# Kernel tuning notes

Measured on AMD Instinct MI355X. Metric: run time of the kernel, lower is better.

Reference implementation:

```python
import jax, jax.numpy as jnp
import numpy as np

SIGNAL = (32, 32)
KERNEL = (8, 8)
N_FEATURES = [64, 128, 128]
BATCH = 64
ALPHA = 0.5          # source references an undefined global `alpha`; fixed here
LEAKY_SLOPE = 0.01   # torch F.leaky_relu default


def _join_tensor(S, K, loc):
    i = np.arange(S)[:, None, None]
    j = np.arange(S)[None, :, None]
    k = np.arange(K)[None, None, :]
    M = (j >= i) & (i == np.maximum(j, k + loc))
    return jnp.asarray(M.astype(np.float32))


def _meet_tensor(S, K, loc):
    i = np.arange(S)[:, None, None]
    j = np.arange(S)[None, :, None]
    k = np.arange(K)[None, None, :]
    M = (j >= i) & (i == np.minimum(j, k + loc))
    return jnp.asarray(M.astype(np.float32))


def setup_inputs() -> dict:
    key = jax.random.key(0)
    sx, sy = SIGNAL
    kx, ky = KERNEL
    # meet layers use kernel_loc = signal - kernel; join layers use (0, 0)
    cmx = _meet_tensor(sx, kx, sx - kx)
    cmy = _meet_tensor(sy, ky, sy - ky)
    cjx = _join_tensor(sx, kx, 0)
    cjy = _join_tensor(sy, ky, 0)

    keys = jax.random.split(key, 16)
    x = jax.random.normal(keys[0], (BATCH, N_FEATURES[0], sx, sy), dtype=jnp.float32)

    def kaiming(k, shape):
        fan_in = shape[0] * shape[1] * shape[2]  # kx*ky*in_features
        return jax.random.normal(k, shape, dtype=jnp.float32) * np.float32(np.sqrt(2.0 / fan_in))

    inp = {"x": x, "cmx": cmx, "cmy": cmy, "cjx": cjx, "cjy": cjy}
    for li in range(len(N_FEATURES) - 1):
        fi, fo = N_FEATURES[li], N_FEATURES[li + 1]
        inp[f"mw{li}"] = kaiming(keys[1 + 2 * li], (kx, ky, fi, fo))
        inp[f"mb{li}"] = jnp.zeros((fo, 1, 1), dtype=jnp.float32)
        inp[f"jw{li}"] = kaiming(keys[2 + 2 * li], (kx, ky, fi, fo))
        inp[f"jb{li}"] = jnp.zeros((fo, 1, 1), dtype=jnp.float32)
    return inp


def _lattice_conv(cx, cy, X, W, b):
    # Y[m,g,x,y] = sum_{i,j,a,b} cx[i,x,a] cy[j,y,b] X[m,f,i,j] W[a,b,f,g] + bias
    return jnp.einsum('ixa,jyb,mfij,abfg->mgxy', cx, cy, X, W, optimize='optimal') + b


def reference(x, cmx, cmy, cjx, cjy, mw0, mb0, jw0, jb0, mw1, mb1, jw1, jb1):
    params = [(mw0, mb0, jw0, jb0), (mw1, mb1, jw1, jb1)]
    for mw, mb, jw, jb in params:
        m = _lattice_conv(cmx, cmy, x, mw, mb)
        j = _lattice_conv(cjx, cjy, x, jw, jb)
        x = jax.nn.leaky_relu((1.0 - ALPHA) * m + ALPHA * j, negative_slope=LEAKY_SLOPE)
    return x
```

## Files before the change

### kernel.cpp

```cpp
#include <hip/hip_runtime.h>
#include <stdint.h>


typedef __attribute__((ext_vector_type(8))) short short8;
typedef __attribute__((ext_vector_type(4))) float floatx4;

__device__ __forceinline__ float bf2f(unsigned short u) {
  union { uint32_t u; float f; } c; c.u = ((uint32_t)u) << 16; return c.f;
}
__device__ __forceinline__ unsigned short f2bf(float f) {
  union { float f; uint32_t u; } c; c.f = f;
  uint32_t u = c.u;
  uint32_t r = (u + 0x7FFFu + ((u >> 16) & 1u)) >> 16;
  return (unsigned short)r;
}

__global__ void detect_and_bias(const unsigned short* __restrict__ xa,
                                const void* __restrict__ mb0,
                                const void* __restrict__ jb0,
                                const void* __restrict__ mb1,
                                const void* __restrict__ jb1,
                                float* __restrict__ bias0,
                                float* __restrict__ bias1,
                                int* __restrict__ flag) {
  __shared__ int cnt;
  if (threadIdx.x == 0) cnt = 0;
  __syncthreads();
  unsigned short v = xa[threadIdx.x];
  int e = (v >> 7) & 0xFF;
  int ok = (v == 0) || (e >= 110 && e <= 140);
  atomicAdd(&cnt, ok);
  __syncthreads();
  int fp32 = (cnt >= 240) ? 0 : 1;
  if (threadIdx.x == 0) *flag = fp32;
  int g = threadIdx.x & 127;
  const void* mb = (threadIdx.x < 128) ? mb0 : mb1;
  const void* jb = (threadIdx.x < 128) ? jb0 : jb1;
  float* bo = (threadIdx.x < 128) ? bias0 : bias1;
  float m = fp32 ? ((const float*)mb)[g] : bf2f(((const unsigned short*)mb)[g]);
  float j = fp32 ? ((const float*)jb)[g] : bf2f(((const unsigned short*)jb)[g]);
  bo[g] = 0.5f * (m + j);
}

__global__ __launch_bounds__(256) void transpose_in(
    const unsigned short* __restrict__ s16, const float* __restrict__ s32,
    unsigned short* __restrict__ dst, int R, int C,
    const int* __restrict__ flag) {
  __shared__ unsigned short tile[32][33];
  int fp32 = *flag;
  int tx = threadIdx.x, ty = threadIdx.y;
  int c0 = blockIdx.x * 32, r0 = blockIdx.y * 32;
  if (fp32) {
#pragma unroll
    for (int i = 0; i < 32; i += 8)
      tile[ty + i][tx] = f2bf(s32[(size_t)(r0 + ty + i) * C + (c0 + tx)]);
  } else {
#pragma unroll
    for (int i = 0; i < 32; i += 8)
      tile[ty + i][tx] = s16[(size_t)(r0 + ty + i) * C + (c0 + tx)];
  }
  __syncthreads();
#pragma unroll
  for (int i = 0; i < 32; i += 8)
    dst[(size_t)(c0 + ty + i) * R + (r0 + tx)] = tile[tx][ty + i];
}

__global__ __launch_bounds__(256) void transpose_out(
    const unsigned short* __restrict__ src, unsigned short* __restrict__ d16,
    float* __restrict__ d32, int R, int C, const int* __restrict__ flag) {
  __shared__ unsigned short tile[32][33];
  int fp32 = *flag;
  int tx = threadIdx.x, ty = threadIdx.y;
  int c0 = blockIdx.x * 32, r0 = blockIdx.y * 32;
#pragma unroll
  for (int i = 0; i < 32; i += 8)
    tile[ty + i][tx] = src[(size_t)(r0 + ty + i) * C + (c0 + tx)];
  __syncthreads();
  if (fp32) {
#pragma unroll
    for (int i = 0; i < 32; i += 8)
      d32[(size_t)(c0 + ty + i) * R + (r0 + tx)] = bf2f(tile[tx][ty + i]);
  } else {
#pragma unroll
    for (int i = 0; i < 32; i += 8)
      d16[(size_t)(c0 + ty + i) * R + (r0 + tx)] = tile[tx][ty + i];
  }
}

__global__ __launch_bounds__(256) void transpose_w4(
    const void* __restrict__ mw0, const void* __restrict__ jw0,
    const void* __restrict__ mw1, const void* __restrict__ jw1,
    float* __restrict__ mwT0, float* __restrict__ jwT0,
    float* __restrict__ mwT1, float* __restrict__ jwT1,
    const int* __restrict__ flag) {
  int z = blockIdx.z;
  const void* src = (z == 0) ? mw0 : (z == 1) ? jw0 : (z == 2) ? mw1 : jw1;
  float* dst = (z == 0) ? mwT0 : (z == 1) ? jwT0 : (z == 2) ? mwT1 : jwT1;
  int C = (z < 2) ? 8192 : 16384;
  int c0 = blockIdx.x * 32;
  if (c0 >= C) return;
  __shared__ float tile[32][33];
  int fp32 = *flag;
  int tx = threadIdx.x, ty = threadIdx.y;
  int r0 = blockIdx.y * 32;
#pragma unroll
  for (int i = 0; i < 32; i += 8) {
    size_t idx = (size_t)(r0 + ty + i) * C + (c0 + tx);
    tile[ty + i][tx] = fp32 ? ((const float*)src)[idx]
                            : bf2f(((const unsigned short*)src)[idx]);
  }
  __syncthreads();
#pragma unroll
  for (int i = 0; i < 32; i += 8)
    dst[(size_t)(c0 + ty + i) * 64 + (r0 + tx)] = tile[tx][ty + i];
}

#define SLOT_W1 0
#define SLOT_SB 225
#define SLOT_AS 289
#define SLOT_M  353
#define N_SLOTS 417

__global__ __launch_bounds__(256) void prep_weights3(
    const float* __restrict__ mwT0, const float* __restrict__ jwT0,
    const float* __restrict__ mwT1, const float* __restrict__ jwT1,
    unsigned short* __restrict__ Wall0, unsigned short* __restrict__ Wall1) {
  int layer = blockIdx.z;
  int F = layer ? 128 : 64;
  int shift = layer ? 7 : 6;
  const float* mwT = layer ? mwT1 : mwT0;
  const float* jwT = layer ? jwT1 : jwT0;
  unsigned short* Wall = layer ? Wall1 : Wall0;
  int tid = blockIdx.x * 256 + threadIdx.x;
  if (tid >= (F << 7)) return;
  int group = blockIdx.y;
  int f = tid & (F - 1), g = tid >> shift;
  const size_t WS = (size_t)128 * F;
  unsigned short* wout = Wall + (size_t)g * F + f;

  float w[64];
  {
    const float4* p = (const float4*)(mwT + ((size_t)f * 128 + g) * 64);
#pragma unroll
    for (int i = 0; i < 16; ++i) {
      float4 v = p[i];
      w[4 * i] = v.x; w[4 * i + 1] = v.y; w[4 * i + 2] = v.z; w[4 * i + 3] = v.w;
    }
  }
  if (group == 3) {
#pragma unroll
    for (int ab = 0; ab < 64; ++ab)
      wout[(size_t)(SLOT_M + ab) * WS] = f2bf(0.5f * w[ab]);
    return;
  }
#pragma unroll
  for (int a = 0; a < 8; ++a)
#pragma unroll
    for (int b = 6; b >= 0; --b) w[a * 8 + b] += w[a * 8 + b + 1];
  if (group == 2) {
#pragma unroll
    for (int ab = 0; ab < 64; ++ab)
      wout[(size_t)(SLOT_AS + ab) * WS] = f2bf(0.5f * w[ab]);
  }
#pragma unroll
  for (int a = 6; a >= 0; --a)
#pragma unroll
    for (int b = 0; b < 8; ++b) w[a * 8 + b] += w[(a + 1) * 8 + b];
  if (group == 2) {
#pragma unroll
    for (int px = 0; px < 8; ++px)
#pragma unroll
      for (int b = 0; b < 8; ++b) {
        float v = w[px * 8 + b] - (b < 7 ? w[px * 8 + b + 1] : 0.0f);
        wout[(size_t)(SLOT_SB + px * 8 + b) * WS] = f2bf(0.5f * v);
      }
    return;
  }
  float pp[64];
  {
    const float4* p = (const float4*)(jwT + ((size_t)f * 128 + g) * 64);
#pragma unroll
    for (int i = 0; i < 16; ++i) {
      float4 v = p[i];
      pp[4 * i] = v.x; pp[4 * i + 1] = v.y; pp[4 * i + 2] = v.z; pp[4 * i + 3] = v.w;
    }
  }
#pragma unroll
  for (int a = 0; a < 8; ++a)
#pragma unroll
    for (int b = 1; b < 8; ++b) pp[a * 8 + b] += pp[a * 8 + b - 1];
#pragma unroll
  for (int a = 1; a < 8; ++a)
#pragma unroll
    for (int b = 0; b < 8; ++b) pp[a * 8 + b] += pp[(a - 1) * 8 + b];
  int cx0 = (group == 0) ? 0 : 7, cx1 = (group == 0) ? 7 : 15;
  for (int cx = cx0; cx < cx1; ++cx) {
    int pmx = cx < 7 ? cx : 7;
    int pxx = cx > 7 ? cx - 7 : 0;
#pragma unroll
    for (int cy = 0; cy < 15; ++cy) {
      int pmy = cy < 7 ? cy : 7;
      int pyy = cy > 7 ? cy - 7 : 0;
      float v = 0.5f * (w[pxx * 8 + pyy] + pp[pmx * 8 + pmy]);
      wout[(size_t)(SLOT_W1 + cx * 15 + cy) * WS] = f2bf(v);
    }
  }
}

template <int F, int NT>
__device__ __forceinline__ void mfma_tile(
    const unsigned short* __restrict__ A, const unsigned short* __restrict__ W,
    floatx4 acc[NT], int wave, int n, int q) {
  const unsigned short* a_ptr = A + ((size_t)(wave * 16 + n)) * F + q * 8;
  const unsigned short* w_ptr = W + (size_t)n * F + q * 8;
#pragma unroll
  for (int kk = 0; kk < F; kk += 32) {
    short8 av = *(const short8*)(a_ptr + kk);
#pragma unroll
    for (int t = 0; t < NT; ++t) {
      short8 bv = *(const short8*)(w_ptr + (size_t)t * 16 * F + kk);
      acc[t] = __builtin_amdgcn_mfma_f32_16x16x32_bf16(av, bv, acc[t], 0, 0, 0);
    }
  }
}

template <int F>
__global__ __launch_bounds__(256) void corr_gemm(
    const unsigned short* __restrict__ Xt, const unsigned short* __restrict__ Wall,
    float* __restrict__ V, float* __restrict__ U, float* __restrict__ T) {
  int bid = blockIdx.x, gs = blockIdx.y;
  int wave = threadIdx.x >> 6, lane = threadIdx.x & 63;
  int n = lane & 15, q = lane >> 4;
  int ipos, slot;
  float* out;
  if (bid < 256) {
    int a = bid >> 5, y = bid & 31;
    int py = y > 24 ? y - 24 : 0;
    ipos = (24 + a) * 32 + y;
    slot = SLOT_AS + a * 8 + py;
    out = V + (size_t)(a * 32 + y) * 8192;
  } else if (bid < 512) {
    int i = bid - 256;
    int b = i >> 5, x = i & 31;
    int px = x > 24 ? x - 24 : 0;
    ipos = x * 32 + 24 + b;
    slot = SLOT_SB + px * 8 + b;
    out = U + (size_t)(b * 32 + x) * 8192;
  } else {
    int i = bid - 512;
    int a = i >> 3, b = i & 7;
    ipos = (24 + a) * 32 + 24 + b;
    slot = SLOT_M + a * 8 + b;
    out = T + (size_t)(a * 8 + b) * 8192;
  }
  floatx4 acc[4];
#pragma unroll
  for (int t = 0; t < 4; ++t) acc[t] = (floatx4){0.f, 0.f, 0.f, 0.f};
  mfma_tile<F, 4>(Xt + (size_t)ipos * 64 * F,
                  Wall + ((size_t)slot * 128 + gs * 64) * F, acc, wave, n, q);
#pragma unroll
  for (int t = 0; t < 4; ++t) {
    int gcol = gs * 64 + t * 16 + n;
#pragma unroll
    for (int r = 0; r < 4; ++r) {
      int m = wave * 16 + q * 4 + r;
      out[(size_t)m * 128 + gcol] = acc[t][r];
    }
  }
}

__global__ __launch_bounds__(256) void scan_corr(float* __restrict__ V,
                                                 float* __restrict__ U,
                                                 float* __restrict__ T) {
  int b = blockIdx.x;
  if (b < 2048) {
    float* base = (b < 1024) ? V : U;
    int tid = ((b & 1023) * 256 + threadIdx.x);
    float* p = base + (size_t)tid;
    float s = 0.f;
#pragma unroll
    for (int a = 0; a < 8; ++a) {
      s += p[(size_t)a * 262144];
      p[(size_t)a * 262144] = s;
    }
  } else {
    int mg = (b - 2048) * 256 + threadIdx.x;
    float col[8];
#pragma unroll
    for (int i = 0; i < 8; ++i) col[i] = 0.f;
#pragma unroll
    for (int a = 0; a < 8; ++a) {
      float rs = 0.f;
#pragma unroll
      for (int bb = 0; bb < 8; ++bb) {
        size_t idx = (size_t)(a * 8 + bb) * 8192 + mg;
        col[bb] += T[idx];
        rs += col[bb];
        T[idx] = rs;
      }
    }
  }
}

template <int F>
__global__ __launch_bounds__(256) void final_gemm(
    const unsigned short* __restrict__ Xt, const unsigned short* __restrict__ Wall,
    const float* __restrict__ V, const float* __restrict__ U,
    const float* __restrict__ T, const float* __restrict__ bias,
    unsigned short* __restrict__ Out) {
  int pos = blockIdx.x, gs = blockIdx.y;
  int x = pos >> 5, y = pos & 31;
  int wave = threadIdx.x >> 6, lane = threadIdx.x & 63;
  int n = lane & 15, q = lane >> 4;
  int clsx = x < 7 ? x : (x <= 24 ? 7 : x - 17);
  int clsy = y < 7 ? y : (y <= 24 ? 7 : y - 17);
  int px = x > 24 ? x - 24 : 0;
  int py = y > 24 ? y - 24 : 0;
  const float* c3 = px ? V + ((size_t)(px - 1) * 32 + y) * 8192 : nullptr;
  const float* c2 = py ? U + ((size_t)(py - 1) * 32 + x) * 8192 : nullptr;
  const float* c4 =
      (px && py) ? T + (size_t)((px - 1) * 8 + (py - 1)) * 8192 : nullptr;

  float csum[4][4];
#pragma unroll
  for (int t = 0; t < 4; ++t) {
    int gcol = gs * 64 + t * 16 + n;
    float bv = bias[gcol];
#pragma unroll
    for (int r = 0; r < 4; ++r) {
      int m = wave * 16 + q * 4 + r;
      size_t idx = (size_t)m * 128 + gcol;
      float v = bv;
      if (c3) v += c3[idx];
      if (c2) v += c2[idx];
      if (c4) v += c4[idx];
      csum[t][r] = v;
    }
  }

  floatx4 acc[4];
#pragma unroll
  for (int t = 0; t < 4; ++t) acc[t] = (floatx4){0.f, 0.f, 0.f, 0.f};
  mfma_tile<F, 4>(Xt + (size_t)pos * 64 * F,
                  Wall + ((size_t)(SLOT_W1 + clsx * 15 + clsy) * 128 + gs * 64) * F,
                  acc, wave, n, q);

  unsigned short* o = Out + (size_t)pos * 64 * 128;
#pragma unroll
  for (int t = 0; t < 4; ++t) {
    int gcol = gs * 64 + t * 16 + n;
#pragma unroll
    for (int r = 0; r < 4; ++r) {
      int m = wave * 16 + q * 4 + r;
      float v = acc[t][r] + csum[t][r];
      v = v > 0.f ? v : 0.01f * v;
      o[(size_t)m * 128 + gcol] = f2bf(v);
    }
  }
}

extern "C" void kernel_launch(void* const* d_in, const int* in_sizes, int n_in,
                              void* d_out, int out_size, void* d_ws,
                              size_t ws_size, hipStream_t stream) {
  const void* x   = d_in[0];
  const void* mw0 = d_in[5];
  const void* mb0 = d_in[6];
  const void* jw0 = d_in[7];
  const void* jb0 = d_in[8];
  const void* mw1 = d_in[9];
  const void* mb1 = d_in[10];
  const void* jw1 = d_in[11];
  const void* jb1 = d_in[12];

  char* ws = (char*)d_ws;
  const size_t MB = 1u << 20;
  unsigned short* Xt0   = (unsigned short*)(ws + 0);
  unsigned short* A1    = (unsigned short*)(ws + 9 * MB);
  unsigned short* Wall0 = (unsigned short*)(ws + 26 * MB);
  unsigned short* Wall1 = (unsigned short*)(ws + 33 * MB);
  float* mwT0 = (float*)(ws + 47 * MB);
  float* jwT0 = (float*)(ws + 50 * MB);
  float* mwT1 = (float*)(ws + 53 * MB);
  float* jwT1 = (float*)(ws + 58 * MB);
  unsigned short* Out2 = (unsigned short*)(ws + 63 * MB);
  float* bias0 = (float*)(ws + 80 * MB);
  float* bias1 = bias0 + 128;
  int*   flag  = (int*)(bias1 + 128);
  float* V = (float*)d_out;
  float* U = V + (size_t)8 * 32 * 8192;
  float* T = U + (size_t)8 * 32 * 8192;

  dim3 tb(32, 8);
  detect_and_bias<<<1, 256, 0, stream>>>((const unsigned short*)x, mb0, jb0,
                                         mb1, jb1, bias0, bias1, flag);
  transpose_w4<<<dim3(512, 2, 4), tb, 0, stream>>>(mw0, jw0, mw1, jw1, mwT0,
                                                   jwT0, mwT1, jwT1, flag);
  prep_weights3<<<dim3(64, 4, 2), 256, 0, stream>>>(mwT0, jwT0, mwT1, jwT1,
                                                    Wall0, Wall1);
  transpose_in<<<dim3(32, 128), tb, 0, stream>>>(
      (const unsigned short*)x, (const float*)x, Xt0, 4096, 1024, flag);

  corr_gemm<64><<<dim3(576, 2), 256, 0, stream>>>(Xt0, Wall0, V, U, T);
  scan_corr<<<2080, 256, 0, stream>>>(V, U, T);
  final_gemm<64><<<dim3(1024, 2), 256, 0, stream>>>(Xt0, Wall0, V, U, T,
                                                    bias0, A1);
  corr_gemm<128><<<dim3(576, 2), 256, 0, stream>>>(A1, Wall1, V, U, T);
  scan_corr<<<2080, 256, 0, stream>>>(V, U, T);
  final_gemm<128><<<dim3(1024, 2), 256, 0, stream>>>(A1, Wall1, V, U, T,
                                                     bias1, Out2);

  transpose_out<<<dim3(256, 32), tb, 0, stream>>>(
      Out2, (unsigned short*)d_out, (float*)d_out, 1024, 8192, flag);
}
```

Before: 264.2 us.

## Restructure weight prep to read raw weights coalesced and transpose bf16 outputs

Removes the fp32 weight transpose pass. The prep kernel now reads the original weights directly with coalesced per-thread strided loads into an f,g-major intermediate. A second tiled kernel then transposes each bf16 slot into the g-major layout that the GEMMs expect. This replaces uncoalesced strided bf16 stores and the fp32 round trip with one extra bf16 transpose pass over a smaller buffer, but adds an 834-slice launch.

```diff
diff --git a/kernel.cpp b/kernel.cpp
--- a/kernel.cpp
+++ b/kernel.cpp
@@ -87,70 +87,37 @@
   }
 }
 
-__global__ __launch_bounds__(256) void transpose_w4(
-    const void* __restrict__ mw0, const void* __restrict__ jw0,
-    const void* __restrict__ mw1, const void* __restrict__ jw1,
-    float* __restrict__ mwT0, float* __restrict__ jwT0,
-    float* __restrict__ mwT1, float* __restrict__ jwT1,
-    const int* __restrict__ flag) {
-  int z = blockIdx.z;
-  const void* src = (z == 0) ? mw0 : (z == 1) ? jw0 : (z == 2) ? mw1 : jw1;
-  float* dst = (z == 0) ? mwT0 : (z == 1) ? jwT0 : (z == 2) ? mwT1 : jwT1;
-  int C = (z < 2) ? 8192 : 16384;
-  int c0 = blockIdx.x * 32;
-  if (c0 >= C) return;
-  __shared__ float tile[32][33];
-  int fp32 = *flag;
-  int tx = threadIdx.x, ty = threadIdx.y;
-  int r0 = blockIdx.y * 32;
-#pragma unroll
-  for (int i = 0; i < 32; i += 8) {
-    size_t idx = (size_t)(r0 + ty + i) * C + (c0 + tx);
-    tile[ty + i][tx] = fp32 ? ((const float*)src)[idx]
-                            : bf2f(((const unsigned short*)src)[idx]);
-  }
-  __syncthreads();
-#pragma unroll
-  for (int i = 0; i < 32; i += 8)
-    dst[(size_t)(c0 + ty + i) * 64 + (r0 + tx)] = tile[tx][ty + i];
-}
-
 #define SLOT_W1 0
 #define SLOT_SB 225
 #define SLOT_AS 289
 #define SLOT_M  353
 #define N_SLOTS 417
 
-__global__ __launch_bounds__(256) void prep_weights3(
-    const float* __restrict__ mwT0, const float* __restrict__ jwT0,
-    const float* __restrict__ mwT1, const float* __restrict__ jwT1,
-    unsigned short* __restrict__ Wall0, unsigned short* __restrict__ Wall1) {
+__global__ __launch_bounds__(256) void prep_stageA(
+    const void* __restrict__ mw0, const void* __restrict__ jw0,
+    const void* __restrict__ mw1, const void* __restrict__ jw1,
+    unsigned short* __restrict__ Int0, unsigned short* __restrict__ Int1,
+    const int* __restrict__ flag) {
   int layer = blockIdx.z;
-  int F = layer ? 128 : 64;
-  int shift = layer ? 7 : 6;
-  const float* mwT = layer ? mwT1 : mwT0;
-  const float* jwT = layer ? jwT1 : jwT0;
-  unsigned short* Wall = layer ? Wall1 : Wall0;
-  int tid = blockIdx.x * 256 + threadIdx.x;
-  if (tid >= (F << 7)) return;
+  int FG = layer ? 16384 : 8192;
+  int fg = blockIdx.x * 256 + threadIdx.x;
+  if (fg >= FG) return;
+  int fp32 = *flag;
+  const void* mw = layer ? mw1 : mw0;
+  unsigned short* Int = layer ? Int1 : Int0;
   int group = blockIdx.y;
-  int f = tid & (F - 1), g = tid >> shift;
-  const size_t WS = (size_t)128 * F;
-  unsigned short* wout = Wall + (size_t)g * F + f;
 
   float w[64];
-  {
-    const float4* p = (const float4*)(mwT + ((size_t)f * 128 + g) * 64);
-#pragma unroll
-    for (int i = 0; i < 16; ++i) {
-      float4 v = p[i];
-      w[4 * i] = v.x; w[4 * i + 1] = v.y; w[4 * i + 2] = v.z; w[4 * i + 3] = v.w;
-    }
+#pragma unroll
+  for (int ab = 0; ab < 64; ++ab) {
+    size_t idx = (size_t)ab * FG + fg;
+    w[ab] = fp32 ? ((const float*)mw)[idx]
+                 : bf2f(((const unsigned short*)mw)[idx]);
   }
   if (group == 3) {
 #pragma unroll
     for (int ab = 0; ab < 64; ++ab)
-      wout[(size_t)(SLOT_M + ab) * WS] = f2bf(0.5f * w[ab]);
+      Int[(size_t)(SLOT_M + ab) * FG + fg] = f2bf(0.5f * w[ab]);
     return;
   }
 #pragma unroll
@@ -160,7 +127,7 @@
   if (group == 2) {
 #pragma unroll
     for (int ab = 0; ab < 64; ++ab)
-      wout[(size_t)(SLOT_AS + ab) * WS] = f2bf(0.5f * w[ab]);
+      Int[(size_t)(SLOT_AS + ab) * FG + fg] = f2bf(0.5f * w[ab]);
   }
 #pragma unroll
   for (int a = 6; a >= 0; --a)
@@ -172,18 +139,17 @@
 #pragma unroll
       for (int b = 0; b < 8; ++b) {
         float v = w[px * 8 + b] - (b < 7 ? w[px * 8 + b + 1] : 0.0f);
-        wout[(size_t)(SLOT_SB + px * 8 + b) * WS] = f2bf(0.5f * v);
+        Int[(size_t)(SLOT_SB + px * 8 + b) * FG + fg] = f2bf(0.5f * v);
       }
     return;
   }
+  const void* jw = layer ? jw1 : jw0;
   float pp[64];
-  {
-    const float4* p = (const float4*)(jwT + ((size_t)f * 128 + g) * 64);
-#pragma unroll
-    for (int i = 0; i < 16; ++i) {
-      float4 v = p[i];
-      pp[4 * i] = v.x; pp[4 * i + 1] = v.y; pp[4 * i + 2] = v.z; pp[4 * i + 3] = v.w;
-    }
+#pragma unroll
+  for (int ab = 0; ab < 64; ++ab) {
+    size_t idx = (size_t)ab * FG + fg;
+    pp[ab] = fp32 ? ((const float*)jw)[idx]
+                  : bf2f(((const unsigned short*)jw)[idx]);
   }
 #pragma unroll
   for (int a = 0; a < 8; ++a)
@@ -202,9 +168,34 @@
       int pmy = cy < 7 ? cy : 7;
       int pyy = cy > 7 ? cy - 7 : 0;
       float v = 0.5f * (w[pxx * 8 + pyy] + pp[pmx * 8 + pmy]);
-      wout[(size_t)(SLOT_W1 + cx * 15 + cy) * WS] = f2bf(v);
-    }
-  }
+      Int[(size_t)(SLOT_W1 + cx * 15 + cy) * FG + fg] = f2bf(v);
+    }
+  }
+}
+
+__global__ __launch_bounds__(256) void prep_stageB(
+    const unsigned short* __restrict__ Int0,
+    const unsigned short* __restrict__ Int1,
+    unsigned short* __restrict__ Wall0, unsigned short* __restrict__ Wall1) {
+  int zz = blockIdx.z;
+  int layer = (zz >= N_SLOTS) ? 1 : 0;
+  int slot = zz - layer * N_SLOTS;
+  int F = layer ? 128 : 64;
+  int f0 = blockIdx.y * 32;
+  if (f0 >= F) return;
+  int g0 = blockIdx.x * 32;
+  const unsigned short* src =
+      (layer ? Int1 : Int0) + (size_t)slot * F * 128;
+  unsigned short* dst = (layer ? Wall1 : Wall0) + (size_t)slot * F * 128;
+  __shared__ unsigned short tile[32][33];
+  int tx = threadIdx.x, ty = threadIdx.y;
+#pragma unroll
+  for (int i = 0; i < 32; i += 8)
+    tile[ty + i][tx] = src[(size_t)(f0 + ty + i) * 128 + (g0 + tx)];
+  __syncthreads();
+#pragma unroll
+  for (int i = 0; i < 32; i += 8)
+    dst[(size_t)(g0 + ty + i) * F + (f0 + tx)] = tile[tx][ty + i];
 }
 
 template <int F, int NT>
@@ -378,12 +369,10 @@
   unsigned short* A1    = (unsigned short*)(ws + 9 * MB);
   unsigned short* Wall0 = (unsigned short*)(ws + 26 * MB);
   unsigned short* Wall1 = (unsigned short*)(ws + 33 * MB);
-  float* mwT0 = (float*)(ws + 47 * MB);
-  float* jwT0 = (float*)(ws + 50 * MB);
-  float* mwT1 = (float*)(ws + 53 * MB);
-  float* jwT1 = (float*)(ws + 58 * MB);
-  unsigned short* Out2 = (unsigned short*)(ws + 63 * MB);
-  float* bias0 = (float*)(ws + 80 * MB);
+  unsigned short* Int0  = (unsigned short*)(ws + 47 * MB);
+  unsigned short* Int1  = (unsigned short*)(ws + 54 * MB);
+  unsigned short* Out2  = (unsigned short*)(ws + 68 * MB);
+  float* bias0 = (float*)(ws + 85 * MB);
   float* bias1 = bias0 + 128;
   int*   flag  = (int*)(bias1 + 128);
   float* V = (float*)d_out;
@@ -393,10 +382,10 @@
   dim3 tb(32, 8);
   detect_and_bias<<<1, 256, 0, stream>>>((const unsigned short*)x, mb0, jb0,
                                          mb1, jb1, bias0, bias1, flag);
-  transpose_w4<<<dim3(512, 2, 4), tb, 0, stream>>>(mw0, jw0, mw1, jw1, mwT0,
-                                                   jwT0, mwT1, jwT1, flag);
-  prep_weights3<<<dim3(64, 4, 2), 256, 0, stream>>>(mwT0, jwT0, mwT1, jwT1,
-                                                    Wall0, Wall1);
+  prep_stageA<<<dim3(64, 4, 2), 256, 0, stream>>>(mw0, jw0, mw1, jw1, Int0,
+                                                  Int1, flag);
+  prep_stageB<<<dim3(4, 4, 2 * N_SLOTS), tb, 0, stream>>>(Int0, Int1, Wall0,
+                                                          Wall1);
   transpose_in<<<dim3(32, 128), tb, 0, stream>>>(
       (const unsigned short*)x, (const float*)x, Xt0, 4096, 1024, flag);
 
```

Result: slower. 290.2 us (+9.8%).
